# Optimization experiments

Hardware: AMD Instinct MI355X
Metric: run time of the kernel (lower is better)

Reference implementation:

```python
import jax, jax.numpy as jnp
import numpy as np

B, S, D = 4, 1024, 1024
H = 16
DK = D // H  # per-head dim_q = dim_k = 64
DFF = 4096
EPS = 1e-5


def _layer_norm(x, g, b):
    m = jnp.mean(x, axis=-1, keepdims=True)
    v = jnp.mean((x - m) ** 2, axis=-1, keepdims=True)
    return (x - m) / jnp.sqrt(v + EPS) * g + b


def setup_inputs() -> dict:
    key = jax.random.key(0)
    ks = jax.random.split(key, 16)
    sd = 1.0 / np.sqrt(D)
    sk = 1.0 / np.sqrt(H * DK)
    sf = 1.0 / np.sqrt(DFF)
    return {
        "src": jax.random.normal(ks[0], (B, S, D), jnp.float32),
        # stacked per-head projections (torch loops over H separate nn.Linear)
        "Wq": jax.random.uniform(ks[1], (H, D, DK), jnp.float32, -sd, sd),
        "bq": jax.random.uniform(ks[2], (H, DK), jnp.float32, -sd, sd),
        "Wk": jax.random.uniform(ks[3], (H, D, DK), jnp.float32, -sd, sd),
        "bk": jax.random.uniform(ks[4], (H, DK), jnp.float32, -sd, sd),
        "Wv": jax.random.uniform(ks[5], (H, D, DK), jnp.float32, -sd, sd),
        "bv": jax.random.uniform(ks[6], (H, DK), jnp.float32, -sd, sd),
        "Wo": jax.random.uniform(ks[7], (H * DK, D), jnp.float32, -sk, sk),
        "bo": jax.random.uniform(ks[8], (D,), jnp.float32, -sk, sk),
        "g1": jnp.ones((D,), jnp.float32),
        "be1": jnp.zeros((D,), jnp.float32),
        "W1": jax.random.uniform(ks[9], (D, DFF), jnp.float32, -sd, sd),
        "b1": jax.random.uniform(ks[10], (DFF,), jnp.float32, -sd, sd),
        "W2": jax.random.uniform(ks[11], (DFF, D), jnp.float32, -sf, sf),
        "b2": jax.random.uniform(ks[12], (D,), jnp.float32, -sf, sf),
        "g2": jnp.ones((D,), jnp.float32),
        "be2": jnp.zeros((D,), jnp.float32),
    }


def reference(src, Wq, bq, Wk, bk, Wv, bv, Wo, bo, g1, be1, W1, b1, W2, b2, g2, be2):
    # multi-head attention (all heads batched via einsum instead of python loop)
    q = jnp.einsum("bsd,hdk->bhsk", src, Wq) + bq[None, :, None, :]
    k = jnp.einsum("bsd,hdk->bhsk", src, Wk) + bk[None, :, None, :]
    v = jnp.einsum("bsd,hdk->bhsk", src, Wv) + bv[None, :, None, :]
    scale = jnp.asarray(DK, src.dtype) ** 0.5  # query.size(-1) ** 0.5
    scores = jnp.einsum("bhsk,bhtk->bhst", q, k) / scale
    attn = jax.nn.softmax(scores, axis=-1)
    o = jnp.einsum("bhst,bhtk->bhsk", attn, v)  # [B,H,S,DK]
    o = o.transpose(0, 2, 1, 3).reshape(src.shape[0], src.shape[1], H * DK)
    attn_out = o @ Wo + bo
    x = _layer_norm(src + attn_out, g1, be1)
    ffn = jax.nn.relu(x @ W1 + b1) @ W2 + b2
    return _layer_norm(x + ffn, g2, be2)
```

## Files before the change

### kernel.cpp

```cpp
#include <hip/hip_runtime.h>
#include <hip/hip_bf16.h>

#define DEV __device__ __forceinline__

typedef __attribute__((ext_vector_type(8))) short bf16x8;
typedef __attribute__((ext_vector_type(4))) float f32x4;
typedef __attribute__((ext_vector_type(4))) short short4v;
typedef __attribute__((ext_vector_type(2))) unsigned uint2v;

DEV short f2bf(float f) {
    union { float f; unsigned u; } x; x.f = f;
    unsigned u = x.u;
    unsigned r = (u + 0x7fffu + ((u >> 16) & 1u)) >> 16;
    return (short)r;
}

DEV float bf2f(short s) {
    union { unsigned u; float f; } x;
    x.u = ((unsigned)(unsigned short)s) << 16;
    return x.f;
}

DEV unsigned cvtpk(float a, float b) {
    unsigned r;
    asm("v_cvt_pk_bf16_f32 %0, %1, %2" : "=v"(r) : "v"(a), "v"(b));
    return r;
}

#define GLD16(g, l)                                                         \
    __builtin_amdgcn_global_load_lds(                                       \
        (const __attribute__((address_space(1))) void*)(g),                 \
        (__attribute__((address_space(3))) void*)(l), 16, 0, 0)

#define WAITV(n) asm volatile("s_waitcnt vmcnt(" #n ")" ::: "memory")
#define SBAR()   asm volatile("s_barrier" ::: "memory")
#define LGKM0()                                              \
    asm volatile("s_waitcnt lgkmcnt(0)" ::: "memory");       \
    __builtin_amdgcn_sched_barrier(0)


__global__ __launch_bounds__(256) void k_cast(const float* __restrict__ in,
                                              short* __restrict__ out, int n4) {
    int i = blockIdx.x * 256 + threadIdx.x;
    if (i >= n4) return;
    float4 v = ((const float4*)in)[i];
    short4v o;
    o[0] = f2bf(v.x); o[1] = f2bf(v.y); o[2] = f2bf(v.z); o[3] = f2bf(v.w);
    ((short4v*)out)[i] = o;
}

__global__ __launch_bounds__(256) void k_tr(const float* __restrict__ in,
                                            short* __restrict__ out,
                                            int R, int C,
                                            long in_hs, long out_hs) {
    in  += (size_t)blockIdx.z * in_hs;
    out += (size_t)blockIdx.z * out_hs;
    __shared__ short tile[64][68];
    const int t = threadIdx.x;
    const int r0 = blockIdx.y * 64, c0 = blockIdx.x * 64;
    const int lr = t >> 4, lc4 = (t & 15) * 4;
#pragma unroll
    for (int it = 0; it < 4; ++it) {
        int r = lr + it * 16;
        float4 v = *(const float4*)(in + (size_t)(r0 + r) * C + c0 + lc4);
        tile[lc4 + 0][r] = f2bf(v.x);
        tile[lc4 + 1][r] = f2bf(v.y);
        tile[lc4 + 2][r] = f2bf(v.z);
        tile[lc4 + 3][r] = f2bf(v.w);
    }
    __syncthreads();
#pragma unroll
    for (int it = 0; it < 4; ++it) {
        int c = lr + it * 16;
        short4v o;
        o[0] = tile[c][lc4 + 0];
        o[1] = tile[c][lc4 + 1];
        o[2] = tile[c][lc4 + 2];
        o[3] = tile[c][lc4 + 3];
        *(short4v*)(out + (size_t)(c0 + c) * R + r0 + lc4) = o;
    }
}

template <int MODE>
__global__ __launch_bounds__(512, 2) void k_gemm8(
    const short* __restrict__ A, const short* __restrict__ BT,
    int K, int NT,
    const float* __restrict__ f0, const float* __restrict__ f1,
    const float* __restrict__ f2,
    void* __restrict__ o0, void* __restrict__ o1, void* __restrict__ o2) {
    __shared__ short lds[2][2][2][128 * 64];
    const int t = threadIdx.x;
    const int w = t >> 6, l = t & 63;
    const int l16 = l & 15, lg = l >> 4;
    const int wm = w >> 2, wn = w & 3;
    const int bn = blockIdx.x, bm = blockIdx.y;
    const int koff = blockIdx.z * NT * 64;
    const short* Ab = A + (size_t)bm * 256 * K + koff;
    const short* Bb = BT + (size_t)bn * 256 * K + koff;
    const int srow = l >> 3;
    const int scol = ((l & 7) ^ srow) * 8;
    const int offk0 = ((0 + lg) ^ (l16 & 7)) * 8;
    const int offk1 = ((4 + lg) ^ (l16 & 7)) * 8;

    f32x4 acc[8][4] = {};

    auto stg = [&](int buf, int op, int h, int kt) {
#pragma unroll
        for (int i = 0; i < 2; ++i) {
            int row = h * 128 + w * 16 + i * 8 + srow;
            GLD16((op ? Bb : Ab) + (size_t)row * K + (size_t)kt * 64 + scol,
                  &lds[buf][op][h][(w * 16 + i * 8) * 64]);
        }
    };

    stg(0, 0, 0, 0); stg(0, 0, 1, 0);
    stg(0, 1, 0, 0); stg(0, 1, 1, 0);
    const int t1p = (NT > 1) ? 1 : 0;
    stg(1, 1, 0, t1p); stg(1, 1, 1, t1p);
    WAITV(4);
    SBAR();

    for (int kt = 0; kt < NT; ++kt) {
        const int cur = kt & 1, nxt = cur ^ 1;
        const int t1 = (kt + 1 < NT) ? kt + 1 : NT - 1;
        const int t2 = (kt + 2 < NT) ? kt + 2 : NT - 1;
        bf16x8 a0[4][2], a1[4][2], b0[2][2], b1[2][2];

#pragma unroll
        for (int m = 0; m < 4; ++m) {
            a0[m][0] = *(const bf16x8*)&lds[cur][0][wm][(m * 16 + l16) * 64 + offk0];
            a0[m][1] = *(const bf16x8*)&lds[cur][0][wm][(m * 16 + l16) * 64 + offk1];
        }
#pragma unroll
        for (int n = 0; n < 2; ++n) {
            int r = (wn & 1) * 64 + n * 16 + l16;
            b0[n][0] = *(const bf16x8*)&lds[cur][1][wn >> 1][r * 64 + offk0];
            b0[n][1] = *(const bf16x8*)&lds[cur][1][wn >> 1][r * 64 + offk1];
        }
        stg(nxt, 0, 0, t1);
        SBAR();
        LGKM0();
        __builtin_amdgcn_s_setprio(1);
#pragma unroll
        for (int m = 0; m < 4; ++m)
#pragma unroll
            for (int n = 0; n < 2; ++n) {
                acc[m][n] = __builtin_amdgcn_mfma_f32_16x16x32_bf16(a0[m][0], b0[n][0], acc[m][n], 0, 0, 0);
                acc[m][n] = __builtin_amdgcn_mfma_f32_16x16x32_bf16(a0[m][1], b0[n][1], acc[m][n], 0, 0, 0);
            }
        __builtin_amdgcn_s_setprio(0);
        SBAR();

#pragma unroll
        for (int n = 0; n < 2; ++n) {
            int r = (wn & 1) * 64 + (n + 2) * 16 + l16;
            b1[n][0] = *(const bf16x8*)&lds[cur][1][wn >> 1][r * 64 + offk0];
            b1[n][1] = *(const bf16x8*)&lds[cur][1][wn >> 1][r * 64 + offk1];
        }
        stg(nxt, 0, 1, t1);
        SBAR();
        LGKM0();
        __builtin_amdgcn_s_setprio(1);
#pragma unroll
        for (int m = 0; m < 4; ++m)
#pragma unroll
            for (int n = 0; n < 2; ++n) {
                acc[m][n + 2] = __builtin_amdgcn_mfma_f32_16x16x32_bf16(a0[m][0], b1[n][0], acc[m][n + 2], 0, 0, 0);
                acc[m][n + 2] = __builtin_amdgcn_mfma_f32_16x16x32_bf16(a0[m][1], b1[n][1], acc[m][n + 2], 0, 0, 0);
            }
        __builtin_amdgcn_s_setprio(0);
        SBAR();

#pragma unroll
        for (int m = 0; m < 4; ++m) {
            a1[m][0] = *(const bf16x8*)&lds[cur][0][wm][((m + 4) * 16 + l16) * 64 + offk0];
            a1[m][1] = *(const bf16x8*)&lds[cur][0][wm][((m + 4) * 16 + l16) * 64 + offk1];
        }
        stg(cur, 1, 0, t2);
        SBAR();
        LGKM0();
        __builtin_amdgcn_s_setprio(1);
#pragma unroll
        for (int m = 0; m < 4; ++m)
#pragma unroll
            for (int n = 0; n < 2; ++n) {
                acc[m + 4][n + 2] = __builtin_amdgcn_mfma_f32_16x16x32_bf16(a1[m][0], b1[n][0], acc[m + 4][n + 2], 0, 0, 0);
                acc[m + 4][n + 2] = __builtin_amdgcn_mfma_f32_16x16x32_bf16(a1[m][1], b1[n][1], acc[m + 4][n + 2], 0, 0, 0);
            }
        __builtin_amdgcn_s_setprio(0);
        SBAR();

        stg(cur, 1, 1, t2);
        SBAR();
        __builtin_amdgcn_s_setprio(1);
#pragma unroll
        for (int m = 0; m < 4; ++m)
#pragma unroll
            for (int n = 0; n < 2; ++n) {
                acc[m + 4][n] = __builtin_amdgcn_mfma_f32_16x16x32_bf16(a1[m][0], b0[n][0], acc[m + 4][n], 0, 0, 0);
                acc[m + 4][n] = __builtin_amdgcn_mfma_f32_16x16x32_bf16(a1[m][1], b0[n][1], acc[m + 4][n], 0, 0, 0);
            }
        __builtin_amdgcn_s_setprio(0);
        WAITV(4);
        SBAR();
    }
    WAITV(0);

    const int N = gridDim.x * 256;
#pragma unroll
    for (int m = 0; m < 8; ++m) {
        int rowbase = bm * 256 + wm * 128 + m * 16 + lg * 4;
#pragma unroll
        for (int n = 0; n < 4; ++n) {
            int col = bn * 256 + wn * 64 + n * 16 + l16;
            if constexpr (MODE == 0) {
                int p = col >> 10, c1 = col & 1023;
                int hh = c1 >> 6, dk = c1 & 63;
                const float* bias = (p == 0) ? f0 : (p == 1) ? f1 : f2;
                float bvl = bias[c1];
                float qs = (p == 0) ? 0.18033688011112042f : 1.0f;
                int b = rowbase >> 10, s = rowbase & 1023;
                if (p == 2) {
                    short4v vv;
#pragma unroll
                    for (int rr = 0; rr < 4; ++rr) vv[rr] = f2bf(acc[m][n][rr] + bvl);
                    *(short4v*)((short*)o2 + (((size_t)(b * 16 + hh) * 64 + dk) << 10) + s) = vv;
                } else {
                    short* dst = (p == 0) ? (short*)o0 : (short*)o1;
#pragma unroll
                    for (int rr = 0; rr < 4; ++rr)
                        dst[(((size_t)(b * 16 + hh) << 10) + s + rr) * 64 + dk] =
                            f2bf((acc[m][n][rr] + bvl) * qs);
                }
            } else if constexpr (MODE == 2) {
                float bvl = f0[col];
#pragma unroll
                for (int rr = 0; rr < 4; ++rr) {
                    size_t idx = (size_t)(rowbase + rr) * N + col;
                    float y = acc[m][n][rr] + bvl;
                    ((short*)o0)[idx] = f2bf(y > 0.f ? y : 0.f);
                }
            } else {
                size_t base =
                    ((size_t)blockIdx.z * (gridDim.y * 256) + rowbase) * N + col;
#pragma unroll
                for (int rr = 0; rr < 4; ++rr)
                    ((short*)o0)[base + (size_t)rr * N] = f2bf(acc[m][n][rr]);
            }
        }
    }
}

__global__ __launch_bounds__(256) void k_gemm_s(
    const short* __restrict__ A, const short* __restrict__ BT, int K,
    const float* __restrict__ f0, const float* __restrict__ resid,
    float* __restrict__ o0) {
    __shared__ short Al[128][72];
    __shared__ short Bl[128][72];
    const int t = threadIdx.x;
    const int l = t & 63, w = t >> 6;
    const int l16 = l & 15, lg = l >> 4;
    const int wm = w >> 1, wn = w & 1;
    const int bn = blockIdx.x, bm = blockIdx.y;
    f32x4 acc[4][4] = {};
    const short* Ab = A + (size_t)bm * 128 * K;
    const short* Bb = BT + (size_t)bn * 128 * K;
    const int sr = t >> 3, sc = (t & 7) * 8;

    for (int k0 = 0; k0 < K; k0 += 64) {
#pragma unroll
        for (int it = 0; it < 4; ++it) {
            int rr = sr + it * 32;
            *(bf16x8*)&Al[rr][sc] = *(const bf16x8*)(Ab + (size_t)rr * K + k0 + sc);
            *(bf16x8*)&Bl[rr][sc] = *(const bf16x8*)(Bb + (size_t)rr * K + k0 + sc);
        }
        __syncthreads();
#pragma unroll
        for (int kk = 0; kk < 2; ++kk) {
            bf16x8 af[4], bfv[4];
#pragma unroll
            for (int i = 0; i < 4; ++i)
                af[i] = *(const bf16x8*)&Al[wm * 64 + i * 16 + l16][kk * 32 + lg * 8];
#pragma unroll
            for (int j = 0; j < 4; ++j)
                bfv[j] = *(const bf16x8*)&Bl[wn * 64 + j * 16 + l16][kk * 32 + lg * 8];
#pragma unroll
            for (int i = 0; i < 4; ++i)
#pragma unroll
                for (int j = 0; j < 4; ++j)
                    acc[i][j] = __builtin_amdgcn_mfma_f32_16x16x32_bf16(
                        af[i], bfv[j], acc[i][j], 0, 0, 0);
        }
        __syncthreads();
    }

    const int N = gridDim.x * 128;
#pragma unroll
    for (int i = 0; i < 4; ++i) {
#pragma unroll
        for (int rr = 0; rr < 4; ++rr) {
            int row = bm * 128 + wm * 64 + i * 16 + lg * 4 + rr;
#pragma unroll
            for (int j = 0; j < 4; ++j) {
                int col = bn * 128 + wn * 64 + j * 16 + l16;
                size_t idx = (size_t)row * N + col;
                o0[idx] = acc[i][j][rr] + f0[col] + resid[idx];
            }
        }
    }
}

__global__ __launch_bounds__(256, 4) void k_attn(const short* __restrict__ Q,
                                                 const short* __restrict__ Kt,
                                                 const short* __restrict__ VT,
                                                 short* __restrict__ O) {
    __shared__ short Kl[2][64 * 64];
    __shared__ short Vl[2][64 * 64];
    __shared__ short Pl[4][16 * 64];
    const int bh = blockIdx.x;
    const int qb = blockIdx.y;
    const int t = threadIdx.x;
    const int w = t >> 6, l = t & 63;
    const int l16 = l & 15, lg = l >> 4;
    const int sw = l16 & 7;
    const int pmask = (l16 & 7) << 1;
    const int srow = l >> 3;
    const int scol = ((l & 7) ^ srow) * 8;

    const short* Qb = Q + ((size_t)bh * 1024 + qb * 64 + w * 16 + l16) * 64 + lg * 8;
    bf16x8 qf0 = *(const bf16x8*)Qb;
    bf16x8 qf1 = *(const bf16x8*)(Qb + 32);

    const short* Kbase = Kt + (size_t)bh * (1024 * 64);
    const short* Vbase = VT + (size_t)bh * (64 * 1024);

    const float THR = 11.5415603f;

    float m = -1e30f, ls = 0.f;
    f32x4 oacc[4] = {};

    auto stage = [&](int buf, int t0) {
#pragma unroll
        for (int it = 0; it < 2; ++it) {
            int roww = w * 16 + it * 8;
            GLD16(Kbase + (size_t)(t0 + roww + srow) * 64 + scol,
                  &Kl[buf][roww * 64]);
            GLD16(Vbase + (size_t)(roww + srow) * 1024 + t0 + scol,
                  &Vl[buf][roww * 64]);
        }
    };

    auto compute = [&](int cur) {
        f32x4 s[4];
#pragma unroll
        for (int n = 0; n < 4; ++n) {
            bf16x8 kf0 = *(const bf16x8*)&Kl[cur][(n * 16 + l16) * 64 + (lg ^ sw) * 8];
            bf16x8 kf1 = *(const bf16x8*)&Kl[cur][(n * 16 + l16) * 64 + ((4 + lg) ^ sw) * 8];
            f32x4 a = {0.f, 0.f, 0.f, 0.f};
            a = __builtin_amdgcn_mfma_f32_16x16x32_bf16(kf0, qf0, a, 0, 0, 0);
            a = __builtin_amdgcn_mfma_f32_16x16x32_bf16(kf1, qf1, a, 0, 0, 0);
            s[n] = a;
        }
        float t0m = fmaxf(fmaxf(s[0][0], s[0][1]), fmaxf(s[0][2], s[0][3]));
        float t1m = fmaxf(fmaxf(s[1][0], s[1][1]), fmaxf(s[1][2], s[1][3]));
        float t2m = fmaxf(fmaxf(s[2][0], s[2][1]), fmaxf(s[2][2], s[2][3]));
        float t3m = fmaxf(fmaxf(s[3][0], s[3][1]), fmaxf(s[3][2], s[3][3]));
        float mx = fmaxf(fmaxf(t0m, t1m), fmaxf(t2m, t3m));
        mx = fmaxf(mx, __shfl_xor(mx, 16));
        mx = fmaxf(mx, __shfl_xor(mx, 32));

        if (__any(mx > m + THR)) {
            float mn = fmaxf(m, mx);
            float al = exp2f(m - mn);
            m = mn;
#pragma unroll
            for (int n = 0; n < 4; ++n)
#pragma unroll
                for (int r = 0; r < 4; ++r) s[n][r] = exp2f(s[n][r] - m);
            float su = (s[0][0] + s[0][1]) + (s[0][2] + s[0][3]);
            su += (s[1][0] + s[1][1]) + (s[1][2] + s[1][3]);
            su += (s[2][0] + s[2][1]) + (s[2][2] + s[2][3]);
            su += (s[3][0] + s[3][1]) + (s[3][2] + s[3][3]);
            su += __shfl_xor(su, 16);
            su += __shfl_xor(su, 32);
            ls = ls * al + su;
#pragma unroll
            for (int r = 0; r < 4; ++r) {
                float alr = __shfl(al, lg * 4 + r);
#pragma unroll
                for (int n = 0; n < 4; ++n) oacc[n][r] *= alr;
            }
        } else {
#pragma unroll
            for (int n = 0; n < 4; ++n)
#pragma unroll
                for (int r = 0; r < 4; ++r) s[n][r] = exp2f(s[n][r] - m);
            float su = (s[0][0] + s[0][1]) + (s[0][2] + s[0][3]);
            su += (s[1][0] + s[1][1]) + (s[1][2] + s[1][3]);
            su += (s[2][0] + s[2][1]) + (s[2][2] + s[2][3]);
            su += (s[3][0] + s[3][1]) + (s[3][2] + s[3][3]);
            su += __shfl_xor(su, 16);
            su += __shfl_xor(su, 32);
            ls += su;
        }
#pragma unroll
        for (int n = 0; n < 4; ++n) {
            uint2v pv;
            pv[0] = cvtpk(s[n][0], s[n][1]);
            pv[1] = cvtpk(s[n][2], s[n][3]);
            int g = (n * 4 + lg) ^ pmask;
            *(uint2v*)((char*)Pl[w] + l16 * 128 + g * 8) = pv;
        }
#pragma unroll
        for (int kk = 0; kk < 2; ++kk) {
            int gp = (8 * kk + 2 * lg) ^ pmask;
            bf16x8 pa = *(const bf16x8*)((const char*)Pl[w] + l16 * 128 + gp * 8);
#pragma unroll
            for (int n = 0; n < 4; ++n) {
                bf16x8 vb = *(const bf16x8*)&Vl[cur][(n * 16 + l16) * 64 +
                                                     ((kk * 4 + lg) ^ sw) * 8];
                oacc[n] = __builtin_amdgcn_mfma_f32_16x16x32_bf16(pa, vb, oacc[n],
                                                                  0, 0, 0);
            }
        }
    };

    stage(0, 0);
    for (int ti = 0; ti < 15; ++ti) {
        int cur = ti & 1;
        stage(cur ^ 1, (ti + 1) * 64);
        WAITV(4);
        SBAR();
        compute(cur);
        SBAR();
    }
    WAITV(0);
    SBAR();
    compute(1);

    const int b = bh >> 4, h = bh & 15;
#pragma unroll
    for (int r = 0; r < 4; ++r) {
        float lsr = __shfl(ls, lg * 4 + r);
        float inv = 1.f / lsr;
        size_t row = (size_t)(b * 1024 + qb * 64 + w * 16 + lg * 4 + r);
#pragma unroll
        for (int n = 0; n < 4; ++n)
            O[row * 1024 + h * 64 + n * 16 + l16] = f2bf(oacc[n][r] * inv);
    }
}

__global__ __launch_bounds__(256) void k_ln(const float* __restrict__ in,
                                            const float* __restrict__ g,
                                            const float* __restrict__ be,
                                            float* __restrict__ of,
                                            short* __restrict__ ob) {
    const int row = blockIdx.x, t = threadIdx.x;
    float4 x = ((const float4*)(in + ((size_t)row << 10)))[t];
    float s = x.x + x.y + x.z + x.w;
    float s2 = x.x * x.x + x.y * x.y + x.z * x.z + x.w * x.w;
#pragma unroll
    for (int mm = 1; mm < 64; mm <<= 1) {
        s += __shfl_xor(s, mm);
        s2 += __shfl_xor(s2, mm);
    }
    __shared__ float red[8];
    if ((t & 63) == 0) { red[t >> 6] = s; red[4 + (t >> 6)] = s2; }
    __syncthreads();
    s = red[0] + red[1] + red[2] + red[3];
    s2 = red[4] + red[5] + red[6] + red[7];
    float mean = s * (1.f / 1024.f);
    float var = s2 * (1.f / 1024.f) - mean * mean;
    float rstd = rsqrtf(var + 1e-5f);
    int c = t * 4;
    float4 y;
    y.x = (x.x - mean) * rstd * g[c + 0] + be[c + 0];
    y.y = (x.y - mean) * rstd * g[c + 1] + be[c + 1];
    y.z = (x.z - mean) * rstd * g[c + 2] + be[c + 2];
    y.w = (x.w - mean) * rstd * g[c + 3] + be[c + 3];
    if (of) ((float4*)(of + ((size_t)row << 10)))[t] = y;
    if (ob) {
        short4v o;
        o[0] = f2bf(y.x); o[1] = f2bf(y.y); o[2] = f2bf(y.z); o[3] = f2bf(y.w);
        ((short4v*)(ob + ((size_t)row << 10)))[t] = o;
    }
}

__global__ __launch_bounds__(256) void k_lnred(const short* __restrict__ part,
                                               const float* __restrict__ bias,
                                               const float* __restrict__ resid,
                                               const float* __restrict__ g,
                                               const float* __restrict__ be,
                                               float* __restrict__ of) {
    const int row = blockIdx.x, t = threadIdx.x;
    float4 x = ((const float4*)(resid + ((size_t)row << 10)))[t];
    float4 bv = ((const float4*)bias)[t];
    x.x += bv.x; x.y += bv.y; x.z += bv.z; x.w += bv.w;
#pragma unroll
    for (int kz = 0; kz < 4; ++kz) {
        short4v p = ((const short4v*)(part + (((size_t)kz * 4096 + row) << 10)))[t];
        x.x += bf2f(p[0]); x.y += bf2f(p[1]); x.z += bf2f(p[2]); x.w += bf2f(p[3]);
    }
    float s = x.x + x.y + x.z + x.w;
    float s2 = x.x * x.x + x.y * x.y + x.z * x.z + x.w * x.w;
#pragma unroll
    for (int mm = 1; mm < 64; mm <<= 1) {
        s += __shfl_xor(s, mm);
        s2 += __shfl_xor(s2, mm);
    }
    __shared__ float red[8];
    if ((t & 63) == 0) { red[t >> 6] = s; red[4 + (t >> 6)] = s2; }
    __syncthreads();
    s = red[0] + red[1] + red[2] + red[3];
    s2 = red[4] + red[5] + red[6] + red[7];
    float mean = s * (1.f / 1024.f);
    float var = s2 * (1.f / 1024.f) - mean * mean;
    float rstd = rsqrtf(var + 1e-5f);
    int c = t * 4;
    float4 y;
    y.x = (x.x - mean) * rstd * g[c + 0] + be[c + 0];
    y.y = (x.y - mean) * rstd * g[c + 1] + be[c + 1];
    y.z = (x.z - mean) * rstd * g[c + 2] + be[c + 2];
    y.w = (x.w - mean) * rstd * g[c + 3] + be[c + 3];
    ((float4*)(of + ((size_t)row << 10)))[t] = y;
}

extern "C" void kernel_launch(void* const* d_in, const int* in_sizes, int n_in,
                              void* d_out, int out_size, void* d_ws, size_t ws_size,
                              hipStream_t stream) {
    (void)in_sizes; (void)n_in; (void)out_size; (void)ws_size;
    const float* src = (const float*)d_in[0];
    const float* Wq  = (const float*)d_in[1];
    const float* bq  = (const float*)d_in[2];
    const float* Wk  = (const float*)d_in[3];
    const float* bk  = (const float*)d_in[4];
    const float* Wv  = (const float*)d_in[5];
    const float* bv  = (const float*)d_in[6];
    const float* Wo  = (const float*)d_in[7];
    const float* bo  = (const float*)d_in[8];
    const float* g1  = (const float*)d_in[9];
    const float* be1 = (const float*)d_in[10];
    const float* W1  = (const float*)d_in[11];
    const float* b1  = (const float*)d_in[12];
    const float* W2  = (const float*)d_in[13];
    const float* b2  = (const float*)d_in[14];
    const float* g2  = (const float*)d_in[15];
    const float* be2 = (const float*)d_in[16];

    char* ws = (char*)d_ws;
    const size_t MB = 1048576;
    short* srcbf = (short*)(ws + 0);
    short* Qb    = (short*)(ws + 8 * MB);
    short* Kb    = (short*)(ws + 16 * MB);
    short* VTb   = (short*)(ws + 24 * MB);
    short* h1    = (short*)(ws + 0);
    short* Obuf  = srcbf;
    short* W2T   = (short*)(ws + 32 * MB);
    float* xf    = (float*)(ws + 40 * MB);
    short* WqkvT = (short*)(ws + 56 * MB);
    short* WoT   = (short*)(ws + 62 * MB);
    short* W1T   = (short*)(ws + 64 * MB);
    float* xres  = (float*)(ws + 72 * MB);
    short* xbf   = (short*)(ws + 88 * MB);
    short* part  = (short*)(ws + 56 * MB);

    k_cast<<<4096, 256, 0, stream>>>(src, srcbf, 1048576);
    k_tr<<<dim3(1, 16, 16), 256, 0, stream>>>(Wq, WqkvT,           1024, 64, 65536, 65536);
    k_tr<<<dim3(1, 16, 16), 256, 0, stream>>>(Wk, WqkvT + 1048576, 1024, 64, 65536, 65536);
    k_tr<<<dim3(1, 16, 16), 256, 0, stream>>>(Wv, WqkvT + 2097152, 1024, 64, 65536, 65536);
    k_tr<<<dim3(16, 16, 1), 256, 0, stream>>>(Wo, WoT, 1024, 1024, 0, 0);
    k_tr<<<dim3(64, 16, 1), 256, 0, stream>>>(W1, W1T, 1024, 4096, 0, 0);
    k_tr<<<dim3(16, 64, 1), 256, 0, stream>>>(W2, W2T, 4096, 1024, 0, 0);
    k_gemm8<0><<<dim3(12, 16, 1), 512, 0, stream>>>(srcbf, WqkvT, 1024, 16,
                                                    bq, bk, bv, Qb, Kb, VTb);
    k_attn<<<dim3(64, 16), 256, 0, stream>>>(Qb, Kb, VTb, Obuf);
    k_gemm_s<<<dim3(8, 32), 256, 0, stream>>>(Obuf, WoT, 1024, bo, src, xres);
    k_ln<<<4096, 256, 0, stream>>>(xres, g1, be1, xf, xbf);
    k_gemm8<2><<<dim3(16, 16, 1), 512, 0, stream>>>(xbf, W1T, 1024, 16,
                                                    b1, nullptr, nullptr,
                                                    h1, nullptr, nullptr);
    k_gemm8<3><<<dim3(4, 16, 4), 512, 0, stream>>>(h1, W2T, 4096, 16,
                                                   nullptr, nullptr, nullptr,
                                                   part, nullptr, nullptr);
    k_lnred<<<4096, 256, 0, stream>>>(part, b2, xf, g2, be2, (float*)d_out);
}
```

Before: 219.6 us.

## Double attention query tile per block and compute softmax row sums via MFMA

The attention kernel now runs 512 threads (8 waves) per block covering 128 query rows, so each K/V tile staged in shared memory serves twice as many queries and the grid is halved. Each wave issues one K and one V load per tile instead of two, and the wait count drops to match. The softmax denominator is no longer built from scalar adds and cross-lane shuffles; it comes from an extra MFMA that multiplies P by a vector of ones. The max reduction is also regrouped. This cuts global K/V traffic and VALU/shuffle work, at the cost of fewer, larger blocks, a larger P buffer in shared memory, and summing P after bf16 rounding.

Result: faster. 214.7 us (-2.2%).

```diff
diff --git a/kernel.cpp b/kernel.cpp
--- a/kernel.cpp
+++ b/kernel.cpp
@@ -310,13 +310,13 @@
     }
 }
 
-__global__ __launch_bounds__(256, 4) void k_attn(const short* __restrict__ Q,
+__global__ __launch_bounds__(512, 4) void k_attn(const short* __restrict__ Q,
                                                  const short* __restrict__ Kt,
                                                  const short* __restrict__ VT,
                                                  short* __restrict__ O) {
     __shared__ short Kl[2][64 * 64];
     __shared__ short Vl[2][64 * 64];
-    __shared__ short Pl[4][16 * 64];
+    __shared__ short Pl[8][16 * 64];
     const int bh = blockIdx.x;
     const int qb = blockIdx.y;
     const int t = threadIdx.x;
@@ -327,7 +327,7 @@
     const int srow = l >> 3;
     const int scol = ((l & 7) ^ srow) * 8;
 
-    const short* Qb = Q + ((size_t)bh * 1024 + qb * 64 + w * 16 + l16) * 64 + lg * 8;
+    const short* Qb = Q + ((size_t)bh * 1024 + qb * 128 + w * 16 + l16) * 64 + lg * 8;
     bf16x8 qf0 = *(const bf16x8*)Qb;
     bf16x8 qf1 = *(const bf16x8*)(Qb + 32);
 
@@ -336,18 +336,20 @@
 
     const float THR = 11.5415603f;
 
-    float m = -1e30f, ls = 0.f;
+    bf16x8 ones;
+#pragma unroll
+    for (int i = 0; i < 8; ++i) ones[i] = (short)0x3F80;
+
+    float m = -1e30f;
     f32x4 oacc[4] = {};
+    f32x4 oaccS = {};
 
     auto stage = [&](int buf, int t0) {
-#pragma unroll
-        for (int it = 0; it < 2; ++it) {
-            int roww = w * 16 + it * 8;
-            GLD16(Kbase + (size_t)(t0 + roww + srow) * 64 + scol,
-                  &Kl[buf][roww * 64]);
-            GLD16(Vbase + (size_t)(roww + srow) * 1024 + t0 + scol,
-                  &Vl[buf][roww * 64]);
-        }
+        int roww = w * 8;
+        GLD16(Kbase + (size_t)(t0 + roww + srow) * 64 + scol,
+              &Kl[buf][roww * 64]);
+        GLD16(Vbase + (size_t)(roww + srow) * 1024 + t0 + scol,
+              &Vl[buf][roww * 64]);
     };
 
     auto compute = [&](int cur) {
@@ -361,11 +363,13 @@
             a = __builtin_amdgcn_mfma_f32_16x16x32_bf16(kf1, qf1, a, 0, 0, 0);
             s[n] = a;
         }
-        float t0m = fmaxf(fmaxf(s[0][0], s[0][1]), fmaxf(s[0][2], s[0][3]));
-        float t1m = fmaxf(fmaxf(s[1][0], s[1][1]), fmaxf(s[1][2], s[1][3]));
-        float t2m = fmaxf(fmaxf(s[2][0], s[2][1]), fmaxf(s[2][2], s[2][3]));
-        float t3m = fmaxf(fmaxf(s[3][0], s[3][1]), fmaxf(s[3][2], s[3][3]));
-        float mx = fmaxf(fmaxf(t0m, t1m), fmaxf(t2m, t3m));
+        float m1 = fmaxf(fmaxf(s[0][0], s[0][1]), s[0][2]);
+        float m2 = fmaxf(fmaxf(s[0][3], s[1][0]), s[1][1]);
+        float m3 = fmaxf(fmaxf(s[1][2], s[1][3]), s[2][0]);
+        float m4 = fmaxf(fmaxf(s[2][1], s[2][2]), s[2][3]);
+        float m5 = fmaxf(fmaxf(s[3][0], s[3][1]), s[3][2]);
+        float mx = fmaxf(fmaxf(m1, m2), m3);
+        mx = fmaxf(fmaxf(m4, m5), fmaxf(mx, s[3][3]));
         mx = fmaxf(mx, __shfl_xor(mx, 16));
         mx = fmaxf(mx, __shfl_xor(mx, 32));
 
@@ -377,16 +381,10 @@
             for (int n = 0; n < 4; ++n)
 #pragma unroll
                 for (int r = 0; r < 4; ++r) s[n][r] = exp2f(s[n][r] - m);
-            float su = (s[0][0] + s[0][1]) + (s[0][2] + s[0][3]);
-            su += (s[1][0] + s[1][1]) + (s[1][2] + s[1][3]);
-            su += (s[2][0] + s[2][1]) + (s[2][2] + s[2][3]);
-            su += (s[3][0] + s[3][1]) + (s[3][2] + s[3][3]);
-            su += __shfl_xor(su, 16);
-            su += __shfl_xor(su, 32);
-            ls = ls * al + su;
 #pragma unroll
             for (int r = 0; r < 4; ++r) {
                 float alr = __shfl(al, lg * 4 + r);
+                oaccS[r] *= alr;
 #pragma unroll
                 for (int n = 0; n < 4; ++n) oacc[n][r] *= alr;
             }
@@ -395,13 +393,6 @@
             for (int n = 0; n < 4; ++n)
 #pragma unroll
                 for (int r = 0; r < 4; ++r) s[n][r] = exp2f(s[n][r] - m);
-            float su = (s[0][0] + s[0][1]) + (s[0][2] + s[0][3]);
-            su += (s[1][0] + s[1][1]) + (s[1][2] + s[1][3]);
-            su += (s[2][0] + s[2][1]) + (s[2][2] + s[2][3]);
-            su += (s[3][0] + s[3][1]) + (s[3][2] + s[3][3]);
-            su += __shfl_xor(su, 16);
-            su += __shfl_xor(su, 32);
-            ls += su;
         }
 #pragma unroll
         for (int n = 0; n < 4; ++n) {
@@ -415,6 +406,7 @@
         for (int kk = 0; kk < 2; ++kk) {
             int gp = (8 * kk + 2 * lg) ^ pmask;
             bf16x8 pa = *(const bf16x8*)((const char*)Pl[w] + l16 * 128 + gp * 8);
+            oaccS = __builtin_amdgcn_mfma_f32_16x16x32_bf16(pa, ones, oaccS, 0, 0, 0);
 #pragma unroll
             for (int n = 0; n < 4; ++n) {
                 bf16x8 vb = *(const bf16x8*)&Vl[cur][(n * 16 + l16) * 64 +
@@ -429,7 +421,7 @@
     for (int ti = 0; ti < 15; ++ti) {
         int cur = ti & 1;
         stage(cur ^ 1, (ti + 1) * 64);
-        WAITV(4);
+        WAITV(2);
         SBAR();
         compute(cur);
         SBAR();
@@ -441,9 +433,8 @@
     const int b = bh >> 4, h = bh & 15;
 #pragma unroll
     for (int r = 0; r < 4; ++r) {
-        float lsr = __shfl(ls, lg * 4 + r);
-        float inv = 1.f / lsr;
-        size_t row = (size_t)(b * 1024 + qb * 64 + w * 16 + lg * 4 + r);
+        float inv = 1.f / oaccS[r];
+        size_t row = (size_t)(b * 1024 + qb * 128 + w * 16 + lg * 4 + r);
 #pragma unroll
         for (int n = 0; n < 4; ++n)
             O[row * 1024 + h * 64 + n * 16 + l16] = f2bf(oacc[n][r] * inv);
@@ -573,7 +564,7 @@
     k_tr<<<dim3(16, 64, 1), 256, 0, stream>>>(W2, W2T, 4096, 1024, 0, 0);
     k_gemm8<0><<<dim3(12, 16, 1), 512, 0, stream>>>(srcbf, WqkvT, 1024, 16,
                                                     bq, bk, bv, Qb, Kb, VTb);
-    k_attn<<<dim3(64, 16), 256, 0, stream>>>(Qb, Kb, VTb, Obuf);
+    k_attn<<<dim3(64, 8), 512, 0, stream>>>(Qb, Kb, VTb, Obuf);
     k_gemm_s<<<dim3(8, 32), 256, 0, stream>>>(Obuf, WoT, 1024, bo, src, xres);
     k_ln<<<4096, 256, 0, stream>>>(xres, g1, be1, xf, xbf);
     k_gemm8<2><<<dim3(16, 16, 1), 512, 0, stream>>>(xbf, W1T, 1024, 16,
```
